# Kernel optimization log

Measured on AMD Instinct MI355X. Metric: run time of the kernel, lower is better.

Reference implementation:

```python
import jax, jax.numpy as jnp
import numpy as np

EPS = 1e-12

def l2norm(v, axis):
    return v / jnp.maximum(jnp.linalg.norm(v, axis=axis, keepdims=True), EPS)

def setup_inputs() -> dict:
    key = jax.random.key(0)
    k1, k2, k3, k4 = jax.random.split(key, 4)
    N, C, S, K = 16, 128, 16384, 64
    return {
        "x": jax.random.normal(k1, (N, C, S), dtype=jnp.float32),
        "fc_w": jax.random.normal(k2, (K, C), dtype=jnp.float32),
        "fc_b": jax.random.normal(k3, (K,), dtype=jnp.float32),
        "centroids": jax.random.uniform(k4, (K, C), dtype=jnp.float32),
    }

def reference(x, fc_w, fc_b, centroids):
    # x: [N, C, S]; fc_w: [K, C]; centroids: [K, C]
    x = l2norm(x, axis=1)  # descriptor-wise L2 normalize over channels
    # 1x1 conv (per-position linear) -> soft assignment over clusters
    logits = jnp.einsum('ncs,kc->nks', x, fc_w) + fc_b[None, :, None]
    soft = jax.nn.softmax(logits, axis=1)  # [N, K, S]
    # vlad[n,k,c] = sum_s soft[n,k,s] * (x[n,c,s] - centroids[k,c])
    # matmul decomposition avoids materializing [N,K,C,S]
    a_sum = soft.sum(axis=-1)  # [N, K]
    vlad = jnp.einsum('nks,ncs->nkc', soft, x) - a_sum[:, :, None] * centroids[None]
    vlad = l2norm(vlad, axis=2)            # intra-normalization
    vlad = vlad.reshape(vlad.shape[0], -1)  # [N, K*C]
    vlad = l2norm(vlad, axis=1)            # final L2 normalize
    return vlad
```

## Files before the change

### kernel.cpp

```cpp
#include <hip/hip_runtime.h>
#include <hip/hip_fp16.h>

#define N_ 16
#define C_ 128
#define S_ 16384
#define K_ 64

typedef __attribute__((ext_vector_type(4))) float f32x4;
typedef __attribute__((ext_vector_type(8))) _Float16 f16x8;
typedef __attribute__((ext_vector_type(4))) _Float16 f16x4;

#define SWZ_S(s) ((((s) ^ ((s) >> 3)) & 7) << 3)
#define SWZ16(k) (((k) & 7) << 3)
#define SWZ8(r) (((r) & 7) << 3)

static __device__ __forceinline__ unsigned int pack_fp8x4(float a, float b,
                                                          float c, float d) {
    int v = __builtin_amdgcn_cvt_pk_fp8_f32(a, b, 0, false);
    v = __builtin_amdgcn_cvt_pk_fp8_f32(c, d, v, true);
    return (unsigned int)v;
}

__global__ __launch_bounds__(256, 3) void fused_kernel(
    const float* __restrict__ x, const float* __restrict__ fc_w,
    const float* __restrict__ fc_b, float* __restrict__ vlad_part,
    float* __restrict__ a_part)
{
    __shared__ __align__(16) _Float16 xT[64 * 128];
    __shared__ __align__(16) _Float16 Wlds[64 * 128];
    __shared__ __align__(16) unsigned char xC8[2][128 * 64];
    __shared__ __align__(16) unsigned char sst8[64 * 64];
    __shared__ float rns[2][64];

    const int tid = threadIdx.x;
    const int lane = tid & 63, w = tid >> 6;
    const int lr = lane & 15, g = lane >> 4;
    const int fsw8 = SWZ8(lr);
    const int fsw16 = SWZ16(lr);

    const int b = blockIdx.x;
    const int n     = (b < 256) ? (b >> 4) : ((b - 256) >> 5);
    const int lo    = (b < 256) ? (b & 15) * 6 : 96 + ((b - 256) & 31) * 5;
    const int cnt   = (b < 256) ? 6 : 5;
    const int jslot = (b < 256) ? (b & 15) : 16 + ((b - 256) & 31);
    const int sl    = n * 48 + jslot;

#pragma unroll
    for (int i = 0; i < 8; ++i) {
        int idx = i * 256 + tid;
        int c4 = idx & 31, k = idx >> 5;
        float4 wv = *(const float4*)(fc_w + k * C_ + c4 * 4);
        f16x4 hi = {(_Float16)wv.x, (_Float16)wv.y, (_Float16)wv.z, (_Float16)wv.w};
        *(f16x4*)&Wlds[k * 128 + ((c4 * 4) ^ SWZ16(k))] = hi;
    }
    if (tid < 128) (&rns[0][0])[tid] = 0.f;

    float bias[4];
#pragma unroll
    for (int nt = 0; nt < 4; ++nt) bias[nt] = fc_b[nt * 16 + lr];
    float a_acc[4] = {0.f, 0.f, 0.f, 0.f};
    f32x4 vacc[8];
#pragma unroll
    for (int nt = 0; nt < 8; ++nt) vacc[nt] = (f32x4){0.f, 0.f, 0.f, 0.f};
    f32x4 accp[4];

    const float* xb = x + (size_t)n * C_ * S_;
    const int s4 = tid & 15;
    int cqv[2];
#pragma unroll
    for (int i = 0; i < 2; ++i) cqv[i] = i * 16 + (tid >> 4);

    float4 pre[2][4];
#pragma unroll
    for (int i = 0; i < 2; ++i)
#pragma unroll
        for (int cc = 0; cc < 4; ++cc)
            pre[i][cc] = *(const float4*)(xb + (size_t)(cqv[i] * 4 + cc) * S_ +
                                          lo * 64 + s4 * 4);

    auto softmax_emit = [&](int pit) {
        float rnl[4], ai[4];
#pragma unroll
        for (int r = 0; r < 4; ++r)
            rnl[r] = 1.0f / fmaxf(sqrtf(rns[pit][w * 16 + g * 4 + r]), 1e-12f);
        if (lane < 16) rns[pit][w * 16 + lane] = 0.f;
#pragma unroll
        for (int nt = 0; nt < 4; ++nt)
#pragma unroll
            for (int r = 0; r < 4; ++r)
                accp[nt][r] = __expf(accp[nt][r] * rnl[r] + bias[nt]);
#pragma unroll
        for (int r = 0; r < 4; ++r) {
            float sum = (accp[0][r] + accp[1][r]) + (accp[2][r] + accp[3][r]);
            sum += __shfl_xor(sum, 1);
            sum += __shfl_xor(sum, 2);
            sum += __shfl_xor(sum, 4);
            sum += __shfl_xor(sum, 8);
            float bi = 1.0f / sum;
            ai[r] = bi * rnl[r] * 256.0f;
#pragma unroll
            for (int nt = 0; nt < 4; ++nt) a_acc[nt] += accp[nt][r] * bi;
        }
#pragma unroll
        for (int nt = 0; nt < 4; ++nt) {
            int k = nt * 16 + lr;
            int sloc = w * 16 + g * 4;
            unsigned int pk = pack_fp8x4(accp[nt][0] * ai[0], accp[nt][1] * ai[1],
                                         accp[nt][2] * ai[2], accp[nt][3] * ai[3]);
            *(unsigned int*)&sst8[k * 64 + (sloc ^ SWZ8(k))] = pk;
        }
    };

#pragma unroll 1
    for (int it = 0; it < cnt; ++it) {
        const int bb = it & 1;
        __syncthreads();

        float part[4] = {0.f, 0.f, 0.f, 0.f};
#pragma unroll
        for (int i = 0; i < 2; ++i) {
            int cq = cqv[i];
#pragma unroll
            for (int jj = 0; jj < 4; ++jj) {
                float v0 = (&pre[i][0].x)[jj], v1 = (&pre[i][1].x)[jj],
                      v2 = (&pre[i][2].x)[jj], v3 = (&pre[i][3].x)[jj];
                part[jj] += v0 * v0 + v1 * v1 + v2 * v2 + v3 * v3;
                f16x4 p = {(_Float16)v0, (_Float16)v1, (_Float16)v2, (_Float16)v3};
                int s = s4 * 4 + jj;
                *(f16x4*)&xT[s * 128 + ((cq * 4) ^ SWZ_S(s))] = p;
            }
#pragma unroll
            for (int cc = 0; cc < 4; ++cc) {
                int c = cq * 4 + cc;
                unsigned int pk = pack_fp8x4(pre[i][cc].x, pre[i][cc].y,
                                             pre[i][cc].z, pre[i][cc].w);
                *(unsigned int*)&xC8[bb][c * 64 + ((s4 * 4) ^ SWZ8(c))] = pk;
            }
        }
#pragma unroll
        for (int jj = 0; jj < 4; ++jj) {
            part[jj] += __shfl_xor(part[jj], 16);
            part[jj] += __shfl_xor(part[jj], 32);
        }
        if (g == 0) {
#pragma unroll
            for (int jj = 0; jj < 4; ++jj)
                atomicAdd(&rns[it & 1][lr * 4 + jj], part[jj]);
        }
        if (it > 0) softmax_emit((it - 1) & 1);
        if (it + 1 < cnt) {
            const float* xb2 = xb + (lo + it + 1) * 64;
#pragma unroll
            for (int i = 0; i < 2; ++i)
#pragma unroll
                for (int cc = 0; cc < 4; ++cc)
                    pre[i][cc] = *(const float4*)(xb2 + (size_t)(cqv[i] * 4 + cc) * S_ + s4 * 4);
        }
        __syncthreads();

#pragma unroll
        for (int nt = 0; nt < 4; ++nt) accp[nt] = (f32x4){0.f, 0.f, 0.f, 0.f};
        __builtin_amdgcn_s_setprio(1);
#pragma unroll
        for (int kt = 0; kt < 4; ++kt) {
            const int co = kt * 32 + g * 8;
            const int sa = w * 16 + lr;
            f16x8 af = *(const f16x8*)&xT[sa * 128 + (co ^ SWZ_S(sa))];
#pragma unroll
            for (int nt = 0; nt < 4; ++nt) {
                f16x8 wf = *(const f16x8*)&Wlds[(nt * 16 + lr) * 128 + (co ^ fsw16)];
                accp[nt] = __builtin_amdgcn_mfma_f32_16x16x32_f16(af, wf, accp[nt], 0, 0, 0);
            }
        }
        if (it > 0) {
            const unsigned char* xcp = xC8[bb ^ 1];
#pragma unroll
            for (int kt = 0; kt < 2; ++kt) {
                const int so = kt * 32 + g * 8;
                long pa = *(const long*)&sst8[(w * 16 + lr) * 64 + (so ^ fsw8)];
#pragma unroll
                for (int nt = 0; nt < 8; ++nt) {
                    long xv = *(const long*)&xcp[(nt * 16 + lr) * 64 + (so ^ fsw8)];
                    vacc[nt] = __builtin_amdgcn_mfma_f32_16x16x32_fp8_fp8(pa, xv, vacc[nt], 0, 0, 0);
                }
            }
        }
        __builtin_amdgcn_s_setprio(0);
    }

    const int lastb = (cnt - 1) & 1;
    __syncthreads();
    softmax_emit(lastb);
    __syncthreads();
    {
        const unsigned char* xcp = xC8[lastb];
#pragma unroll
        for (int kt = 0; kt < 2; ++kt) {
            const int so = kt * 32 + g * 8;
            long pa = *(const long*)&sst8[(w * 16 + lr) * 64 + (so ^ fsw8)];
#pragma unroll
            for (int nt = 0; nt < 8; ++nt) {
                long xv = *(const long*)&xcp[(nt * 16 + lr) * 64 + (so ^ fsw8)];
                vacc[nt] = __builtin_amdgcn_mfma_f32_16x16x32_fp8_fp8(pa, xv, vacc[nt], 0, 0, 0);
            }
        }
    }

    float* vp = vlad_part + (size_t)sl * (K_ * C_) + (w * 16) * C_;
#pragma unroll
    for (int nt = 0; nt < 8; ++nt)
#pragma unroll
        for (int r = 0; r < 4; ++r)
            vp[(g * 4 + r) * C_ + nt * 16 + lr] = vacc[nt][r] * (1.0f / 256.0f);
#pragma unroll
    for (int nt = 0; nt < 4; ++nt) {
        a_acc[nt] += __shfl_xor(a_acc[nt], 16);
        a_acc[nt] += __shfl_xor(a_acc[nt], 32);
    }
    if (lane < 16) {
#pragma unroll
        for (int nt = 0; nt < 4; ++nt)
            a_part[sl * 256 + w * 64 + nt * 16 + lr] = a_acc[nt];
    }
}

__global__ __launch_bounds__(256) void reduce_kernel(
    const float* __restrict__ vlad_part, float* __restrict__ vlad_sum)
{
    const int n = blockIdx.x >> 5, g8 = blockIdx.x & 31;
    const int e = g8 * 256 + threadIdx.x;
    const float* p = vlad_part + (size_t)(n * 48) * (K_ * C_) + e;
    float acc = 0.f;
#pragma unroll
    for (int jj = 0; jj < 48; ++jj) acc += p[(size_t)jj * (K_ * C_)];
    vlad_sum[n * (K_ * C_) + e] = acc;
}

__global__ __launch_bounds__(1024) void finalize_kernel(
    const float* __restrict__ vlad_sum, const float* __restrict__ a_part,
    const float* __restrict__ centroids, float* __restrict__ out)
{
    __shared__ float red[16];
    const int n = blockIdx.x;
    const int t = threadIdx.x;
    const int k = t >> 4, q = t & 15;

    float av = 0.f;
#pragma unroll
    for (int cc = 0; cc < 3; ++cc) {
        int ch = q * 3 + cc;
        const float* ap = a_part + (size_t)(n * 48 + ch) * 256 + k;
#pragma unroll
        for (int ww = 0; ww < 4; ++ww) av += ap[ww * 64];
    }
    av += __shfl_xor(av, 1);
    av += __shfl_xor(av, 2);
    av += __shfl_xor(av, 4);
    av += __shfl_xor(av, 8);

    const float* vp = vlad_sum + (size_t)n * (K_ * C_) + k * C_;
    const float* cp = centroids + k * C_;
    float v[8];
    float ssq = 0.f;
#pragma unroll
    for (int jj = 0; jj < 8; ++jj) {
        int c = q + 16 * jj;
        float val = vp[c] - av * cp[c];
        v[jj] = val;
        ssq += val * val;
    }
    ssq += __shfl_xor(ssq, 1);
    ssq += __shfl_xor(ssq, 2);
    ssq += __shfl_xor(ssq, 4);
    ssq += __shfl_xor(ssq, 8);
    const float inv1 = 1.0f / fmaxf(sqrtf(ssq), 1e-12f);

    float gp = (q == 0) ? ssq * inv1 * inv1 : 0.f;
#pragma unroll
    for (int off = 1; off < 64; off <<= 1) gp += __shfl_xor(gp, off);
    if ((t & 63) == 0) red[t >> 6] = gp;
    __syncthreads();
    float G = 0.f;
#pragma unroll
    for (int i = 0; i < 16; ++i) G += red[i];
    const float ginv = 1.0f / fmaxf(sqrtf(G), 1e-12f);

    float* op = out + (size_t)n * (K_ * C_) + k * C_;
#pragma unroll
    for (int jj = 0; jj < 8; ++jj) op[q + 16 * jj] = v[jj] * inv1 * ginv;
}

extern "C" void kernel_launch(void* const* d_in, const int* in_sizes, int n_in,
                              void* d_out, int out_size, void* d_ws, size_t ws_size,
                              hipStream_t stream) {
    const float* x     = (const float*)d_in[0];
    const float* fc_w  = (const float*)d_in[1];
    const float* fc_b  = (const float*)d_in[2];
    const float* cent  = (const float*)d_in[3];
    float* out = (float*)d_out;

    char* ws = (char*)d_ws;
    float* vlad_part = (float*)ws;
    float* a_part    = (float*)(ws + (size_t)768 * K_ * C_ * 4);
    float* vlad_sum  = (float*)(ws + (size_t)768 * K_ * C_ * 4 + 786432);

    fused_kernel<<<768, 256, 0, stream>>>(x, fc_w, fc_b, vlad_part, a_part);
    reduce_kernel<<<512, 256, 0, stream>>>(vlad_part, vlad_sum);
    finalize_kernel<<<N_, 1024, 0, stream>>>(vlad_sum, a_part, cent, out);
}
```

Measured before the change: 51.52 us.

## Store fp16 partials, fuse reduction into finalize, and issue prefetch earlier

```diff
diff --git a/kernel.cpp b/kernel.cpp
--- a/kernel.cpp
+++ b/kernel.cpp
@@ -23,7 +23,7 @@
 
 __global__ __launch_bounds__(256, 3) void fused_kernel(
     const float* __restrict__ x, const float* __restrict__ fc_w,
-    const float* __restrict__ fc_b, float* __restrict__ vlad_part,
+    const float* __restrict__ fc_b, __half* __restrict__ vlad_part,
     float* __restrict__ a_part)
 {
     __shared__ __align__(16) _Float16 xT[64 * 128];
@@ -137,6 +137,14 @@
                 *(unsigned int*)&xC8[bb][c * 64 + ((s4 * 4) ^ SWZ8(c))] = pk;
             }
         }
+        if (it + 1 < cnt) {
+            const float* xb2 = xb + (lo + it + 1) * 64;
+#pragma unroll
+            for (int i = 0; i < 2; ++i)
+#pragma unroll
+                for (int cc = 0; cc < 4; ++cc)
+                    pre[i][cc] = *(const float4*)(xb2 + (size_t)(cqv[i] * 4 + cc) * S_ + s4 * 4);
+        }
 #pragma unroll
         for (int jj = 0; jj < 4; ++jj) {
             part[jj] += __shfl_xor(part[jj], 16);
@@ -148,14 +156,6 @@
                 atomicAdd(&rns[it & 1][lr * 4 + jj], part[jj]);
         }
         if (it > 0) softmax_emit((it - 1) & 1);
-        if (it + 1 < cnt) {
-            const float* xb2 = xb + (lo + it + 1) * 64;
-#pragma unroll
-            for (int i = 0; i < 2; ++i)
-#pragma unroll
-                for (int cc = 0; cc < 4; ++cc)
-                    pre[i][cc] = *(const float4*)(xb2 + (size_t)(cqv[i] * 4 + cc) * S_ + s4 * 4);
-        }
         __syncthreads();
 
 #pragma unroll
@@ -206,12 +206,13 @@
         }
     }
 
-    float* vp = vlad_part + (size_t)sl * (K_ * C_) + (w * 16) * C_;
+    __half* vp = vlad_part + (size_t)sl * (K_ * C_) + (w * 16) * C_;
 #pragma unroll
     for (int nt = 0; nt < 8; ++nt)
 #pragma unroll
         for (int r = 0; r < 4; ++r)
-            vp[(g * 4 + r) * C_ + nt * 16 + lr] = vacc[nt][r] * (1.0f / 256.0f);
+            vp[(g * 4 + r) * C_ + nt * 16 + lr] =
+                __float2half(vacc[nt][r] * (1.0f / 256.0f));
 #pragma unroll
     for (int nt = 0; nt < 4; ++nt) {
         a_acc[nt] += __shfl_xor(a_acc[nt], 16);
@@ -224,26 +225,26 @@
     }
 }
 
-__global__ __launch_bounds__(256) void reduce_kernel(
-    const float* __restrict__ vlad_part, float* __restrict__ vlad_sum)
-{
-    const int n = blockIdx.x >> 5, g8 = blockIdx.x & 31;
-    const int e = g8 * 256 + threadIdx.x;
-    const float* p = vlad_part + (size_t)(n * 48) * (K_ * C_) + e;
-    float acc = 0.f;
-#pragma unroll
-    for (int jj = 0; jj < 48; ++jj) acc += p[(size_t)jj * (K_ * C_)];
-    vlad_sum[n * (K_ * C_) + e] = acc;
-}
-
 __global__ __launch_bounds__(1024) void finalize_kernel(
-    const float* __restrict__ vlad_sum, const float* __restrict__ a_part,
+    const __half* __restrict__ vlad_part, const float* __restrict__ a_part,
     const float* __restrict__ centroids, float* __restrict__ out)
 {
     __shared__ float red[16];
     const int n = blockIdx.x;
     const int t = threadIdx.x;
     const int k = t >> 4, q = t & 15;
+    const int c0 = q * 8;
+
+    float vsum[8] = {0.f, 0.f, 0.f, 0.f, 0.f, 0.f, 0.f, 0.f};
+    {
+        const __half* p = vlad_part + (size_t)(n * 48) * (K_ * C_) + k * C_ + c0;
+#pragma unroll 4
+        for (int slb = 0; slb < 48; ++slb) {
+            f16x8 v = *(const f16x8*)(p + (size_t)slb * (K_ * C_));
+#pragma unroll
+            for (int jj = 0; jj < 8; ++jj) vsum[jj] += (float)v[jj];
+        }
+    }
 
     float av = 0.f;
 #pragma unroll
@@ -258,14 +259,15 @@
     av += __shfl_xor(av, 4);
     av += __shfl_xor(av, 8);
 
-    const float* vp = vlad_sum + (size_t)n * (K_ * C_) + k * C_;
-    const float* cp = centroids + k * C_;
+    const float* cp = centroids + k * C_ + c0;
+    float4 cpa = *(const float4*)cp;
+    float4 cpb = *(const float4*)(cp + 4);
     float v[8];
     float ssq = 0.f;
 #pragma unroll
     for (int jj = 0; jj < 8; ++jj) {
-        int c = q + 16 * jj;
-        float val = vp[c] - av * cp[c];
+        float cv = (jj < 4) ? (&cpa.x)[jj] : (&cpb.x)[jj - 4];
+        float val = vsum[jj] - av * cv;
         v[jj] = val;
         ssq += val * val;
     }
@@ -285,9 +287,15 @@
     for (int i = 0; i < 16; ++i) G += red[i];
     const float ginv = 1.0f / fmaxf(sqrtf(G), 1e-12f);
 
-    float* op = out + (size_t)n * (K_ * C_) + k * C_;
-#pragma unroll
-    for (int jj = 0; jj < 8; ++jj) op[q + 16 * jj] = v[jj] * inv1 * ginv;
+    float* op = out + (size_t)n * (K_ * C_) + k * C_ + c0;
+    float4 oa, ob;
+#pragma unroll
+    for (int jj = 0; jj < 4; ++jj) {
+        (&oa.x)[jj] = v[jj] * inv1 * ginv;
+        (&ob.x)[jj] = v[jj + 4] * inv1 * ginv;
+    }
+    *(float4*)op = oa;
+    *(float4*)(op + 4) = ob;
 }
 
 extern "C" void kernel_launch(void* const* d_in, const int* in_sizes, int n_in,
@@ -300,11 +308,9 @@
     float* out = (float*)d_out;
 
     char* ws = (char*)d_ws;
-    float* vlad_part = (float*)ws;
-    float* a_part    = (float*)(ws + (size_t)768 * K_ * C_ * 4);
-    float* vlad_sum  = (float*)(ws + (size_t)768 * K_ * C_ * 4 + 786432);
+    __half* vlad_part = (__half*)ws;
+    float* a_part     = (float*)(ws + (size_t)768 * K_ * C_ * 2);
 
     fused_kernel<<<768, 256, 0, stream>>>(x, fc_w, fc_b, vlad_part, a_part);
-    reduce_kernel<<<512, 256, 0, stream>>>(vlad_part, vlad_sum);
-    finalize_kernel<<<N_, 1024, 0, stream>>>(vlad_sum, a_part, cent, out);
+    finalize_kernel<<<N_, 1024, 0, stream>>>(vlad_part, a_part, cent, out);
 }
```

After: 57.92 us. 12.4% more time.
